# Kernel tuning notes

Hardware: AMD Instinct MI355X
Metric: run time of the kernel (lower is better)

The kernel has to match this reference:

```python
import jax, jax.numpy as jnp
import numpy as np

N_NODES, N_EDGES = 16384, 8192
IN_CH, HID_CH = 256, 256
ALPHA, BETA = -1.5, -0.5


def setup_inputs() -> dict:
    key = jax.random.key(0)
    k1, k2, k3, k4, k5, k6 = jax.random.split(key, 6)
    x_0 = jax.random.normal(k1, (N_NODES, IN_CH), dtype=jnp.float32)
    # binary incidence matrix (n_nodes, n_edges)
    incidence_1 = jax.random.randint(k2, (N_NODES, N_EDGES), 0, 2).astype(jnp.float32)
    # conv weights (torch Conv: x @ W then neighborhood @ .)
    W0 = jax.random.normal(k3, (IN_CH, HID_CH), dtype=jnp.float32) * 0.02
    W1 = jax.random.normal(k4, (HID_CH, HID_CH), dtype=jnp.float32) * 0.02
    # xavier_uniform biases of shape (1, hidden)
    gain = 1.414
    bound = gain * np.sqrt(6.0 / (1 + HID_CH)) * np.sqrt(3.0) / np.sqrt(3.0)  # xavier bound = gain*sqrt(6/(fan_in+fan_out))
    bound = gain * np.sqrt(6.0 / (1 + HID_CH))
    bias_0_to_1 = jax.random.uniform(k5, (1, HID_CH), minval=-bound, maxval=bound, dtype=jnp.float32)
    bias_1_to_0 = jax.random.uniform(k6, (1, HID_CH), minval=-bound, maxval=bound, dtype=jnp.float32)
    return {"x_0": x_0, "incidence_1": incidence_1, "W0": W0, "W1": W1,
            "bias_0_to_1": bias_0_to_1, "bias_1_to_0": bias_1_to_0}


def _normalize_incidence(B1):
    # edge/node cardinalities raised to alpha/beta
    edge_card = jnp.sum(B1, axis=0) ** ALPHA          # (n_edges,)
    node_card = jnp.sum(B1, axis=1) ** BETA           # (n_nodes,)
    mask = (B1 > 0).astype(B1.dtype)
    d0_inv = 1.0 / (mask @ edge_card)                 # (n_nodes,) per-node sum of incident edge_card
    d1_inv = 1.0 / (mask.T @ node_card)               # (n_edges,) per-edge sum of member node_card
    # B1_norm = D0_left^-1 @ B1 @ diag(edge_card)
    B1_norm = d0_inv[:, None] * B1 * edge_card[None, :]
    # B1T_norm = D1_left^-1 @ B1^T @ diag(node_card)
    B1T_norm = d1_inv[:, None] * B1.T * node_card[None, :]
    return B1_norm, B1T_norm


def reference(x_0, incidence_1, W0, W1, bias_0_to_1, bias_1_to_0):
    B1_norm, B1T_norm = _normalize_incidence(incidence_1)
    # node -> edge conv: x_1 = B1T_norm @ (x_0 @ W0) + b01
    x_1 = B1T_norm @ (x_0 @ W0) + bias_0_to_1        # (n_edges, hid)
    # edge -> node conv: x_0 = B1_norm @ (x_1 @ W1) + b10
    x_0_out = B1_norm @ (x_1 @ W1) + bias_1_to_0     # (n_nodes, hid)
    return jax.nn.relu(x_0_out), jax.nn.relu(x_1)
```

## Files before the change

kernel.cpp:

```cpp
#include <hip/hip_runtime.h>
#include <stdint.h>

#define NN 16384
#define NE 8192
#define CH 256
#define MM1_SPLIT 8
#define MM2_SPLIT 4

typedef __attribute__((ext_vector_type(8))) short bf16x8;
typedef __attribute__((ext_vector_type(4))) float f32x4;

__device__ __forceinline__ unsigned short f2bf(float f) {
  unsigned u = __float_as_uint(f);
  u += 0x7FFFu + ((u >> 16) & 1u);
  return (unsigned short)(u >> 16);
}
__device__ __forceinline__ unsigned pack_trunc2(float a, float b) {
  return (__float_as_uint(b) & 0xFFFF0000u) | (__float_as_uint(a) >> 16);
}
__device__ __forceinline__ void async_copy16(const void* gptr, void* lptr) {
  __builtin_amdgcn_global_load_lds((const __attribute__((address_space(1))) unsigned int*)gptr,
                                   (__attribute__((address_space(3))) unsigned int*)lptr,
                                   16, 0, 0);
}

__global__ void k0_transpose_w(const float* __restrict__ W0, const float* __restrict__ W1,
                               unsigned short* __restrict__ W0T, unsigned short* __restrict__ W1T) {
  const float* W = blockIdx.y ? W1 : W0;
  unsigned short* WT = blockIdx.y ? W1T : W0T;
  int n = blockIdx.x;
  int k = threadIdx.x;
  WT[n * CH + k] = f2bf(W[k * CH + n]);
}

__global__ void k0z_zero(float* __restrict__ rowsum) {
  rowsum[blockIdx.x * 256 + threadIdx.x] = 0.f;
}

__global__ __launch_bounds__(256) void k1_prep(const float* __restrict__ B1,
                                               unsigned short* __restrict__ b1h,
                                               unsigned short* __restrict__ b1hT,
                                               float* __restrict__ rowsum) {
  __shared__ unsigned short t16[128 * 136];
  __shared__ float rs[128][9];
  const int tid = threadIdx.x;
  const int e0 = blockIdx.x * 128;
  const int n0 = blockIdx.y * 128;
  const int rr = tid >> 3;
  const int ec = (tid & 7) * 16;
  float part[4];
#pragma unroll
  for (int rg = 0; rg < 4; ++rg) {
    int r = rg * 32 + rr;
    const float* src = B1 + (size_t)(n0 + r) * NE + e0 + ec;
    float s = 0.f;
    unsigned w[8];
#pragma unroll
    for (int u = 0; u < 4; ++u) {
      float4 v = *(const float4*)(src + u * 4);
      s += v.x + v.y + v.z + v.w;
      w[u * 2] = pack_trunc2(v.x, v.y);
      w[u * 2 + 1] = pack_trunc2(v.z, v.w);
    }
    part[rg] = s;
    uint4* d = (uint4*)(b1h + (size_t)(n0 + r) * NE + e0 + ec);
    d[0] = make_uint4(w[0], w[1], w[2], w[3]);
    d[1] = make_uint4(w[4], w[5], w[6], w[7]);
    unsigned* lp = (unsigned*)&t16[r * 136 + ec];
#pragma unroll
    for (int u = 0; u < 8; ++u) lp[u] = w[u];
  }
#pragma unroll
  for (int rg = 0; rg < 4; ++rg) rs[rg * 32 + rr][tid & 7] = part[rg];
  __syncthreads();
  if (tid < 128) {
    float s = 0.f;
#pragma unroll
    for (int u = 0; u < 8; ++u) s += rs[tid][u];
    atomicAdd(rowsum + n0 + tid, s);
  }
  const int p = tid & 63, h = tid >> 6;
  unsigned lo[16], hi[16];
#pragma unroll
  for (int u = 0; u < 16; ++u) {
    int n = h * 32 + u * 2;
    unsigned a = *(const unsigned*)&t16[n * 136 + p * 2];
    unsigned b = *(const unsigned*)&t16[(n + 1) * 136 + p * 2];
    lo[u] = (a & 0xFFFFu) | (b << 16);
    hi[u] = (a >> 16) | (b & 0xFFFF0000u);
  }
  uint4* d0 = (uint4*)(b1hT + (size_t)(e0 + 2 * p) * NN + n0 + h * 32);
  d0[0] = make_uint4(lo[0], lo[1], lo[2], lo[3]);
  d0[1] = make_uint4(lo[4], lo[5], lo[6], lo[7]);
  d0[2] = make_uint4(lo[8], lo[9], lo[10], lo[11]);
  d0[3] = make_uint4(lo[12], lo[13], lo[14], lo[15]);
  uint4* d1 = (uint4*)(b1hT + (size_t)(e0 + 2 * p + 1) * NN + n0 + h * 32);
  d1[0] = make_uint4(hi[0], hi[1], hi[2], hi[3]);
  d1[1] = make_uint4(hi[4], hi[5], hi[6], hi[7]);
  d1[2] = make_uint4(hi[8], hi[9], hi[10], hi[11]);
  d1[3] = make_uint4(hi[12], hi[13], hi[14], hi[15]);
}

__global__ void k1b_nc(const float* __restrict__ rowsum, float* __restrict__ node_card) {
  int n = blockIdx.x * 256 + threadIdx.x;
  node_card[n] = rsqrtf(rowsum[n]);
}

__global__ __launch_bounds__(256) void k2_y0(const float* __restrict__ X0,
                                             const unsigned short* __restrict__ W0T,
                                             const float* __restrict__ node_card,
                                             unsigned short* __restrict__ y0sT) {
  __shared__ unsigned short a_lds[64 * 32];
  __shared__ unsigned short b_lds[256 * 32];
  const int tid = threadIdx.x;
  const int wave = tid >> 6, lane = tid & 63;
  const int quad = lane >> 4, l15 = lane & 15;
  const int m0 = blockIdx.x * 64;
  const int ar = tid >> 3, ac = (tid & 7) * 4;

  f32x4 acc[4][4];
  const f32x4 fz = {0.f, 0.f, 0.f, 0.f};
#pragma unroll
  for (int i = 0; i < 4; ++i)
#pragma unroll
    for (int j = 0; j < 4; ++j) acc[i][j] = fz;

  for (int k0 = 0; k0 < CH; k0 += 32) {
    __syncthreads();
#pragma unroll
    for (int p = 0; p < 2; ++p) {
      float4 v = *(const float4*)(X0 + (size_t)(m0 + ar + p * 32) * CH + k0 + ac);
      uint2 w;
      w.x = ((unsigned)f2bf(v.x)) | ((unsigned)f2bf(v.y) << 16);
      w.y = ((unsigned)f2bf(v.z)) | ((unsigned)f2bf(v.w) << 16);
      *(uint2*)&a_lds[(ar + p * 32) * 32 + ac] = w;
    }
#pragma unroll
    for (int i = 0; i < 4; ++i) {
      int rowbase = wave * 64 + i * 16;
      const unsigned short* g = W0T + (size_t)(rowbase + (lane >> 2)) * CH + k0 + (lane & 3) * 8;
      async_copy16(g, &b_lds[rowbase * 32]);
    }
    __syncthreads();
    bf16x8 af[4];
#pragma unroll
    for (int i = 0; i < 4; ++i)
      af[i] = *(const bf16x8*)&a_lds[(i * 16 + l15) * 32 + quad * 8];
#pragma unroll
    for (int j = 0; j < 4; ++j) {
      bf16x8 bfr = *(const bf16x8*)&b_lds[(wave * 64 + j * 16 + l15) * 32 + quad * 8];
#pragma unroll
      for (int i = 0; i < 4; ++i)
        acc[i][j] = __builtin_amdgcn_mfma_f32_16x16x32_bf16(af[i], bfr, acc[i][j], 0, 0, 0);
    }
  }
#pragma unroll
  for (int i = 0; i < 4; ++i) {
    int row4 = m0 + i * 16 + quad * 4;
    float4 nc = *(const float4*)(node_card + row4);
#pragma unroll
    for (int j = 0; j < 4; ++j) {
      int col = wave * 64 + j * 16 + l15;
      f32x4 v = acc[i][j];
      ushort4 o;
      o.x = f2bf(v[0] * nc.x);
      o.y = f2bf(v[1] * nc.y);
      o.z = f2bf(v[2] * nc.z);
      o.w = f2bf(v[3] * nc.w);
      *(ushort4*)&y0sT[(size_t)col * NN + row4] = o;
    }
  }
}

__global__ void k2b_aux(const float* __restrict__ node_card, unsigned short* __restrict__ y0sT) {
  int n = blockIdx.x * 256 + threadIdx.x;
  y0sT[(size_t)256 * NN + n] = f2bf(node_card[n]);
  y0sT[(size_t)257 * NN + n] = 0x3F80;
#pragma unroll
  for (int r = 258; r < 272; ++r) y0sT[(size_t)r * NN + n] = 0;
}

template <int NSZ, int SPLIT>
__device__ __forceinline__ void mm_core(const unsigned short* __restrict__ Y,
                                        const unsigned short* __restrict__ Bm,
                                        float* __restrict__ outp) {
  constexpr int K = (NSZ == NE) ? NN : NE;
  constexpr int KS = K / SPLIT;
  constexpr int ITERS = KS / 64;
  __shared__ unsigned short a_lds[2][2][80][32];
  __shared__ unsigned short b_lds[2][2][128][32];
  const int tid = threadIdx.x;
  const int wave = tid >> 6, lane = tid & 63;
  const int quad = lane >> 4, l15 = lane & 15;
  const int bid = blockIdx.x;
  const int sp = bid % SPLIT;
  const int rest = bid / SPLIT;
  const int mq = rest & 3;
  const int nb = rest >> 2;
  const int n0 = nb * 128;
  const int mbase = mq * 64;
  const int MQ = (mq == 3) ? 5 : 4;
  const int kbase = sp * KS;
  const int lrow = lane >> 2;
  const int src_off = (((lane & 3) - ((lane >> 3) & 3)) & 3) * 8;
  const int qpos = (quad + ((l15 >> 1) & 3)) & 3;

  f32x4 acc[5][2];
  const f32x4 fz = {0.f, 0.f, 0.f, 0.f};
#pragma unroll
  for (int m = 0; m < 5; ++m)
#pragma unroll
    for (int j = 0; j < 2; ++j) acc[m][j] = fz;

  auto stage = [&](int buf, int k0) {
    for (int g = wave; g < MQ; g += 4) {
#pragma unroll
      for (int kh = 0; kh < 2; ++kh) {
        const unsigned short* src =
            Y + (size_t)(mbase + g * 16 + lrow) * K + k0 + kh * 32 + src_off;
        async_copy16(src, &a_lds[buf][kh][g * 16][0]);
      }
    }
#pragma unroll
    for (int gg = 0; gg < 2; ++gg) {
      int g = wave * 2 + gg;
#pragma unroll
      for (int kh = 0; kh < 2; ++kh) {
        const unsigned short* src =
            Bm + (size_t)(n0 + g * 16 + lrow) * K + k0 + kh * 32 + src_off;
        async_copy16(src, &b_lds[buf][kh][g * 16][0]);
      }
    }
  };

  stage(0, kbase);
  for (int i = 0; i < ITERS; ++i) {
    __syncthreads();
    if (i + 1 < ITERS) stage((i + 1) & 1, kbase + (i + 1) * 64);
    const int buf = i & 1;
#pragma unroll
    for (int kh = 0; kh < 2; ++kh) {
      bf16x8 af[5], bfr[2];
#pragma unroll
      for (int m = 0; m < 5; ++m)
        if (m < MQ) af[m] = *(const bf16x8*)&a_lds[buf][kh][m * 16 + l15][qpos * 8];
#pragma unroll
      for (int j = 0; j < 2; ++j)
        bfr[j] = *(const bf16x8*)&b_lds[buf][kh][wave * 32 + j * 16 + l15][qpos * 8];
#pragma unroll
      for (int m = 0; m < 5; ++m)
        if (m < MQ)
#pragma unroll
          for (int j = 0; j < 2; ++j)
            acc[m][j] = __builtin_amdgcn_mfma_f32_16x16x32_bf16(af[m], bfr[j], acc[m][j], 0, 0, 0);
    }
  }
  float* op = outp + (size_t)sp * 272 * NSZ;
#pragma unroll
  for (int m = 0; m < 5; ++m) {
    if (m < MQ) {
      int c0 = mbase + m * 16 + quad * 4;
#pragma unroll
      for (int j = 0; j < 2; ++j) {
        int n = n0 + wave * 32 + j * 16 + l15;
#pragma unroll
        for (int r = 0; r < 4; ++r) op[(size_t)(c0 + r) * NSZ + n] = acc[m][j][r];
      }
    }
  }
}

__global__ __launch_bounds__(256) void mm1t_kernel(const unsigned short* __restrict__ y0sT,
                                                   const unsigned short* __restrict__ b1hT,
                                                   float* __restrict__ mm1pT) {
  mm_core<NE, MM1_SPLIT>(y0sT, b1hT, mm1pT);
}
__global__ __launch_bounds__(256) void mm2t_kernel(const unsigned short* __restrict__ y1sT,
                                                   const unsigned short* __restrict__ b1h,
                                                   float* __restrict__ mm2pT) {
  mm_core<NN, MM2_SPLIT>(y1sT, b1h, mm2pT);
}

__global__ __launch_bounds__(256) void k3_edge_final(const float* __restrict__ mm1pT,
                                                     const float* __restrict__ b01,
                                                     float* __restrict__ out1,
                                                     unsigned short* __restrict__ x1bf,
                                                     float* __restrict__ edge_card) {
  __shared__ float tile[32 * 260];
  __shared__ float d1s[32], css[32];
  const int tid = threadIdx.x;
  const int e0 = blockIdx.x * 32;
  float p[32];
#pragma unroll
  for (int u = 0; u < 32; ++u) p[u] = 0.f;
  for (int sp = 0; sp < MM1_SPLIT; ++sp) {
    const float4* rp = (const float4*)(mm1pT + ((size_t)sp * 272 + tid) * NE + e0);
#pragma unroll
    for (int u = 0; u < 8; ++u) {
      float4 v = rp[u];
      p[u * 4 + 0] += v.x; p[u * 4 + 1] += v.y; p[u * 4 + 2] += v.z; p[u * 4 + 3] += v.w;
    }
  }
  if (tid < 64) {
    int row = 256 + (tid >> 5), e = e0 + (tid & 31);
    float s = 0.f;
    for (int sp = 0; sp < MM1_SPLIT; ++sp) s += mm1pT[((size_t)sp * 272 + row) * NE + e];
    if (tid < 32) d1s[tid] = s; else css[tid & 31] = s;
  }
  __syncthreads();
  float bc = b01[tid];
#pragma unroll
  for (int u = 0; u < 32; ++u) tile[u * 260 + tid] = p[u] / d1s[u] + bc;
  if (tid < 32) {
    float cs = css[tid];
    edge_card[e0 + tid] = 1.0f / (cs * sqrtf(cs));
  }
  __syncthreads();
  const int e = tid >> 3, cb = (tid & 7) * 32;
  const float* trow = &tile[e * 260 + cb];
  float* orow = out1 + (size_t)(e0 + e) * CH + cb;
  unsigned short* xrow = x1bf + (size_t)(e0 + e) * CH + cb;
#pragma unroll
  for (int v = 0; v < 32; v += 4) {
    float4 x;
    x.x = trow[v]; x.y = trow[v + 1]; x.z = trow[v + 2]; x.w = trow[v + 3];
    float4 rl;
    rl.x = fmaxf(x.x, 0.f); rl.y = fmaxf(x.y, 0.f); rl.z = fmaxf(x.z, 0.f); rl.w = fmaxf(x.w, 0.f);
    *(float4*)&orow[v] = rl;
    ushort4 h;
    h.x = f2bf(x.x); h.y = f2bf(x.y); h.z = f2bf(x.z); h.w = f2bf(x.w);
    *(ushort4*)&xrow[v] = h;
  }
}

__global__ __launch_bounds__(256) void k5_y1(const unsigned short* __restrict__ x1bf,
                                             const unsigned short* __restrict__ W1T,
                                             const float* __restrict__ edge_card,
                                             unsigned short* __restrict__ y1sT) {
  __shared__ unsigned short a_lds[64 * 32];
  __shared__ unsigned short b_lds[256 * 32];
  const int tid = threadIdx.x;
  const int wave = tid >> 6, lane = tid & 63;
  const int quad = lane >> 4, l15 = lane & 15;
  const int m0 = blockIdx.x * 64;

  f32x4 acc[4][4];
  const f32x4 fz = {0.f, 0.f, 0.f, 0.f};
#pragma unroll
  for (int i = 0; i < 4; ++i)
#pragma unroll
    for (int j = 0; j < 4; ++j) acc[i][j] = fz;

  for (int k0 = 0; k0 < CH; k0 += 32) {
    __syncthreads();
    {
      const unsigned short* g = x1bf + (size_t)(m0 + wave * 16 + (lane >> 2)) * CH + k0 + (lane & 3) * 8;
      async_copy16(g, &a_lds[(wave * 16) * 32]);
    }
#pragma unroll
    for (int i = 0; i < 4; ++i) {
      int rowbase = wave * 64 + i * 16;
      const unsigned short* g = W1T + (size_t)(rowbase + (lane >> 2)) * CH + k0 + (lane & 3) * 8;
      async_copy16(g, &b_lds[rowbase * 32]);
    }
    __syncthreads();
    bf16x8 af[4];
#pragma unroll
    for (int i = 0; i < 4; ++i)
      af[i] = *(const bf16x8*)&a_lds[(i * 16 + l15) * 32 + quad * 8];
#pragma unroll
    for (int j = 0; j < 4; ++j) {
      bf16x8 bfr = *(const bf16x8*)&b_lds[(wave * 64 + j * 16 + l15) * 32 + quad * 8];
#pragma unroll
      for (int i = 0; i < 4; ++i)
        acc[i][j] = __builtin_amdgcn_mfma_f32_16x16x32_bf16(af[i], bfr, acc[i][j], 0, 0, 0);
    }
  }
#pragma unroll
  for (int i = 0; i < 4; ++i) {
    int row4 = m0 + i * 16 + quad * 4;
    float4 ec = *(const float4*)(edge_card + row4);
#pragma unroll
    for (int j = 0; j < 4; ++j) {
      int col = wave * 64 + j * 16 + l15;
      f32x4 v = acc[i][j];
      ushort4 o;
      o.x = f2bf(v[0] * ec.x);
      o.y = f2bf(v[1] * ec.y);
      o.z = f2bf(v[2] * ec.z);
      o.w = f2bf(v[3] * ec.w);
      *(ushort4*)&y1sT[(size_t)col * NE + row4] = o;
    }
  }
}

__global__ void k5b_aux(const float* __restrict__ edge_card, unsigned short* __restrict__ y1sT) {
  int e = blockIdx.x * 256 + threadIdx.x;
  y1sT[(size_t)256 * NE + e] = f2bf(edge_card[e]);
#pragma unroll
  for (int r = 257; r < 272; ++r) y1sT[(size_t)r * NE + e] = 0;
}

__global__ __launch_bounds__(256) void k6_node_final(const float* __restrict__ mm2pT,
                                                     const float* __restrict__ b10,
                                                     float* __restrict__ out0) {
  __shared__ float tile[32 * 260];
  __shared__ float d0s[32];
  const int tid = threadIdx.x;
  const int n0 = blockIdx.x * 32;
  float p[32];
#pragma unroll
  for (int u = 0; u < 32; ++u) p[u] = 0.f;
  for (int sp = 0; sp < MM2_SPLIT; ++sp) {
    const float4* rp = (const float4*)(mm2pT + ((size_t)sp * 272 + tid) * NN + n0);
#pragma unroll
    for (int u = 0; u < 8; ++u) {
      float4 v = rp[u];
      p[u * 4 + 0] += v.x; p[u * 4 + 1] += v.y; p[u * 4 + 2] += v.z; p[u * 4 + 3] += v.w;
    }
  }
  if (tid < 32) {
    float s = 0.f;
    for (int sp = 0; sp < MM2_SPLIT; ++sp) s += mm2pT[((size_t)sp * 272 + 256) * NN + n0 + tid];
    d0s[tid] = s;
  }
  __syncthreads();
  float bc = b10[tid];
#pragma unroll
  for (int u = 0; u < 32; ++u) tile[u * 260 + tid] = p[u] / d0s[u] + bc;
  __syncthreads();
  const int n = tid >> 3, cb = (tid & 7) * 32;
  const float* trow = &tile[n * 260 + cb];
  float* orow = out0 + (size_t)(n0 + n) * CH + cb;
#pragma unroll
  for (int v = 0; v < 32; v += 4) {
    float4 x;
    x.x = trow[v]; x.y = trow[v + 1]; x.z = trow[v + 2]; x.w = trow[v + 3];
    float4 rl;
    rl.x = fmaxf(x.x, 0.f); rl.y = fmaxf(x.y, 0.f); rl.z = fmaxf(x.z, 0.f); rl.w = fmaxf(x.w, 0.f);
    *(float4*)&orow[v] = rl;
  }
}

extern "C" void kernel_launch(void* const* d_in, const int* in_sizes, int n_in,
                              void* d_out, int out_size, void* d_ws, size_t ws_size,
                              hipStream_t stream) {
  const float* x0 = (const float*)d_in[0];
  const float* B1 = (const float*)d_in[1];
  const float* W0 = (const float*)d_in[2];
  const float* W1 = (const float*)d_in[3];
  const float* b01 = (const float*)d_in[4];
  const float* b10 = (const float*)d_in[5];
  float* out0 = (float*)d_out;
  float* out1 = out0 + (size_t)NN * CH;

  char* ws = (char*)d_ws;
  size_t off = 0;
  auto take = [&](size_t bytes) {
    void* p = ws + off;
    off += (bytes + 255) & ~(size_t)255;
    return p;
  };
  unsigned short* b1h = (unsigned short*)take((size_t)NN * NE * 2);
  unsigned short* b1hT = (unsigned short*)take((size_t)NN * NE * 2);
  unsigned short* y0sT = (unsigned short*)take((size_t)272 * NN * 2);
  unsigned short* y1sT = (unsigned short*)take((size_t)272 * NE * 2);
  unsigned short* x1bf = (unsigned short*)take((size_t)NE * CH * 2);
  float* mm1pT = (float*)take((size_t)MM1_SPLIT * 272 * NE * 4);
  float* mm2pT = mm1pT;
  float* rowsum = (float*)take((size_t)NN * 4);
  float* node_card = (float*)take((size_t)NN * 4);
  float* edge_card = (float*)take((size_t)NE * 4);
  unsigned short* W0T = (unsigned short*)take((size_t)CH * CH * 2);
  unsigned short* W1T = (unsigned short*)take((size_t)CH * CH * 2);
  (void)ws_size; (void)in_sizes; (void)n_in; (void)out_size;

  k0_transpose_w<<<dim3(256, 2), 256, 0, stream>>>(W0, W1, W0T, W1T);
  k0z_zero<<<NN / 256, 256, 0, stream>>>(rowsum);
  k1_prep<<<dim3(NE / 128, NN / 128), 256, 0, stream>>>(B1, b1h, b1hT, rowsum);
  k1b_nc<<<NN / 256, 256, 0, stream>>>(rowsum, node_card);
  k2_y0<<<NN / 64, 256, 0, stream>>>(x0, W0T, node_card, y0sT);
  k2b_aux<<<NN / 256, 256, 0, stream>>>(node_card, y0sT);
  mm1t_kernel<<<(NE / 128) * 4 * MM1_SPLIT, 256, 0, stream>>>(y0sT, b1hT, mm1pT);
  k3_edge_final<<<NE / 32, 256, 0, stream>>>(mm1pT, b01, out1, x1bf, edge_card);
  k5_y1<<<NE / 64, 256, 0, stream>>>(x1bf, W1T, edge_card, y1sT);
  k5b_aux<<<NE / 256, 256, 0, stream>>>(edge_card, y1sT);
  mm2t_kernel<<<(NN / 128) * 4 * MM2_SPLIT, 256, 0, stream>>>(y1sT, b1h, mm2pT);
  k6_node_final<<<NN / 32, 256, 0, stream>>>(mm2pT, b10, out0);
}
```

Measured before the change: 1.148 ms.

## Load matmul operands straight to registers and read fp32 incidence directly in mm2

The LDS-staged matmul core is replaced by a register-prefetching version in which each wave loads its A and B fragments straight from global memory, with 2- and 4-deep prefetch. Tiles grow to 128 or 144 output channels and the split-K factors are halved. mm2 now reads the original fp32 incidence matrix and truncates it to bf16 in registers, so the bf16 copy b1h no longer has to be written. Small kernels are also folded away: the rowsum zeroing moves into the weight transpose and the rsqrt is computed inline. The risks are uncoalesced fragment loads, mm2 reading twice the bytes for B, and higher register pressure.

```diff
diff --git a/kernel.cpp b/kernel.cpp
--- a/kernel.cpp
+++ b/kernel.cpp
@@ -4,8 +4,8 @@
 #define NN 16384
 #define NE 8192
 #define CH 256
-#define MM1_SPLIT 8
-#define MM2_SPLIT 4
+#define MM1_SPLIT 4
+#define MM2_SPLIT 2
 
 typedef __attribute__((ext_vector_type(8))) short bf16x8;
 typedef __attribute__((ext_vector_type(4))) float f32x4;
@@ -25,20 +25,17 @@
 }
 
 __global__ void k0_transpose_w(const float* __restrict__ W0, const float* __restrict__ W1,
-                               unsigned short* __restrict__ W0T, unsigned short* __restrict__ W1T) {
+                               unsigned short* __restrict__ W0T, unsigned short* __restrict__ W1T,
+                               float* __restrict__ rowsum) {
   const float* W = blockIdx.y ? W1 : W0;
   unsigned short* WT = blockIdx.y ? W1T : W0T;
   int n = blockIdx.x;
   int k = threadIdx.x;
   WT[n * CH + k] = f2bf(W[k * CH + n]);
-}
-
-__global__ void k0z_zero(float* __restrict__ rowsum) {
-  rowsum[blockIdx.x * 256 + threadIdx.x] = 0.f;
+  if (blockIdx.y == 0 && blockIdx.x < NN / 256) rowsum[blockIdx.x * 256 + threadIdx.x] = 0.f;
 }
 
 __global__ __launch_bounds__(256) void k1_prep(const float* __restrict__ B1,
-                                               unsigned short* __restrict__ b1h,
                                                unsigned short* __restrict__ b1hT,
                                                float* __restrict__ rowsum) {
   __shared__ unsigned short t16[128 * 136];
@@ -63,9 +60,6 @@
       w[u * 2 + 1] = pack_trunc2(v.z, v.w);
     }
     part[rg] = s;
-    uint4* d = (uint4*)(b1h + (size_t)(n0 + r) * NE + e0 + ec);
-    d[0] = make_uint4(w[0], w[1], w[2], w[3]);
-    d[1] = make_uint4(w[4], w[5], w[6], w[7]);
     unsigned* lp = (unsigned*)&t16[r * 136 + ec];
 #pragma unroll
     for (int u = 0; u < 8; ++u) lp[u] = w[u];
@@ -101,14 +95,9 @@
   d1[3] = make_uint4(hi[12], hi[13], hi[14], hi[15]);
 }
 
-__global__ void k1b_nc(const float* __restrict__ rowsum, float* __restrict__ node_card) {
-  int n = blockIdx.x * 256 + threadIdx.x;
-  node_card[n] = rsqrtf(rowsum[n]);
-}
-
 __global__ __launch_bounds__(256) void k2_y0(const float* __restrict__ X0,
                                              const unsigned short* __restrict__ W0T,
-                                             const float* __restrict__ node_card,
+                                             const float* __restrict__ rowsum,
                                              unsigned short* __restrict__ y0sT) {
   __shared__ unsigned short a_lds[64 * 32];
   __shared__ unsigned short b_lds[256 * 32];
@@ -157,7 +146,9 @@
 #pragma unroll
   for (int i = 0; i < 4; ++i) {
     int row4 = m0 + i * 16 + quad * 4;
-    float4 nc = *(const float4*)(node_card + row4);
+    float4 rsv = *(const float4*)(rowsum + row4);
+    float4 nc;
+    nc.x = rsqrtf(rsv.x); nc.y = rsqrtf(rsv.y); nc.z = rsqrtf(rsv.z); nc.w = rsqrtf(rsv.w);
 #pragma unroll
     for (int j = 0; j < 4; ++j) {
       int col = wave * 64 + j * 16 + l15;
@@ -172,113 +163,137 @@
   }
 }
 
-__global__ void k2b_aux(const float* __restrict__ node_card, unsigned short* __restrict__ y0sT) {
+__global__ void k2b_aux(const float* __restrict__ rowsum, unsigned short* __restrict__ y0sT) {
   int n = blockIdx.x * 256 + threadIdx.x;
-  y0sT[(size_t)256 * NN + n] = f2bf(node_card[n]);
+  y0sT[(size_t)256 * NN + n] = f2bf(rsqrtf(rowsum[n]));
   y0sT[(size_t)257 * NN + n] = 0x3F80;
 #pragma unroll
   for (int r = 258; r < 272; ++r) y0sT[(size_t)r * NN + n] = 0;
 }
 
-template <int NSZ, int SPLIT>
-__device__ __forceinline__ void mm_core(const unsigned short* __restrict__ Y,
-                                        const unsigned short* __restrict__ Bm,
-                                        float* __restrict__ outp) {
-  constexpr int K = (NSZ == NE) ? NN : NE;
+template <int K, int NSZ, int SPLIT, bool F32S>
+__device__ __forceinline__ void mm_core_reg(const unsigned short* __restrict__ Y,
+                                            const void* __restrict__ BmV,
+                                            float* __restrict__ outp,
+                                            int sp, int mb, int nb) {
   constexpr int KS = K / SPLIT;
-  constexpr int ITERS = KS / 64;
-  __shared__ unsigned short a_lds[2][2][80][32];
-  __shared__ unsigned short b_lds[2][2][128][32];
+  constexpr int STEPS = KS / 32;
   const int tid = threadIdx.x;
   const int wave = tid >> 6, lane = tid & 63;
   const int quad = lane >> 4, l15 = lane & 15;
+  const int TM = mb ? 8 : 9, mtb = mb ? 9 : 0;
+  const int n0 = nb * 128 + wave * 32;
+  const int kb0 = sp * KS;
+  const char* Yb = (const char*)Y;
+  const char* Bb = (const char*)BmV;
+
+  f32x4 acc[9][2];
+  const f32x4 fz = {0.f, 0.f, 0.f, 0.f};
+#pragma unroll
+  for (int i = 0; i < 9; ++i)
+#pragma unroll
+    for (int j = 0; j < 2; ++j) acc[i][j] = fz;
+
+  unsigned voffA[9];
+#pragma unroll
+  for (int i = 0; i < 9; ++i)
+    voffA[i] = (unsigned)(((mtb + i) * 16 + l15) * K) * 2u + quad * 16;
+  unsigned voffB[2];
+#pragma unroll
+  for (int j = 0; j < 2; ++j) {
+    unsigned row = (unsigned)(n0 + j * 16 + l15);
+    voffB[j] = F32S ? (row * (unsigned)K * 4u + quad * 32) : (row * (unsigned)K * 2u + quad * 16);
+  }
+
+  bf16x8 Ar[2][9];
+  float4 Brf[4][2][2];
+  bf16x8 Brh[4][2];
+
+  auto loadA = [&](int it, int slot) {
+    unsigned kb = (unsigned)(kb0 + it * 32) * 2u;
+#pragma unroll
+    for (int i = 0; i < 9; ++i)
+      if (i < TM) Ar[slot][i] = *(const bf16x8*)(Yb + voffA[i] + kb);
+  };
+  auto loadB = [&](int it, int slot) {
+    if constexpr (F32S) {
+      unsigned kb = (unsigned)(kb0 + it * 32) * 4u;
+#pragma unroll
+      for (int j = 0; j < 2; ++j) {
+        Brf[slot][j][0] = *(const float4*)(Bb + voffB[j] + kb);
+        Brf[slot][j][1] = *(const float4*)(Bb + voffB[j] + kb + 16);
+      }
+    } else {
+      unsigned kb = (unsigned)(kb0 + it * 32) * 2u;
+#pragma unroll
+      for (int j = 0; j < 2; ++j) Brh[slot][j] = *(const bf16x8*)(Bb + voffB[j] + kb);
+    }
+  };
+
+#pragma unroll
+  for (int p = 0; p < 4; ++p) loadB(p, p);
+#pragma unroll
+  for (int p = 0; p < 2; ++p) loadA(p, p);
+
+#pragma unroll 4
+  for (int it = 0; it < STEPS; ++it) {
+    const int as = it & 1, bs = it & 3;
+#pragma unroll
+    for (int j = 0; j < 2; ++j) {
+      bf16x8 bj;
+      if constexpr (F32S) {
+        const unsigned* u = (const unsigned*)&Brf[bs][j][0];
+        unsigned w[4];
+        w[0] = (u[0] >> 16) | (u[1] & 0xFFFF0000u);
+        w[1] = (u[2] >> 16) | (u[3] & 0xFFFF0000u);
+        w[2] = (u[4] >> 16) | (u[5] & 0xFFFF0000u);
+        w[3] = (u[6] >> 16) | (u[7] & 0xFFFF0000u);
+        bj = *(const bf16x8*)w;
+      } else {
+        bj = Brh[bs][j];
+      }
+#pragma unroll
+      for (int i = 0; i < 9; ++i)
+        if (i < TM) acc[i][j] = __builtin_amdgcn_mfma_f32_16x16x32_bf16(Ar[as][i], bj, acc[i][j], 0, 0, 0);
+    }
+    int ita = it + 2; if (ita >= STEPS) ita = STEPS - 1;
+    loadA(ita, as);
+    int itb = it + 4; if (itb >= STEPS) itb = STEPS - 1;
+    loadB(itb, bs);
+  }
+
+  float* op = outp + (size_t)sp * 272 * NSZ;
+#pragma unroll
+  for (int i = 0; i < 9; ++i) {
+    if (i < TM) {
+      int c0 = (mtb + i) * 16 + quad * 4;
+#pragma unroll
+      for (int j = 0; j < 2; ++j) {
+        int n = n0 + j * 16 + l15;
+#pragma unroll
+        for (int r = 0; r < 4; ++r) op[(size_t)(c0 + r) * NSZ + n] = acc[i][j][r];
+      }
+    }
+  }
+}
+
+__global__ __launch_bounds__(256, 2) void mm1t_kernel(const unsigned short* __restrict__ y0sT,
+                                                      const unsigned short* __restrict__ b1hT,
+                                                      float* __restrict__ mm1pT) {
   const int bid = blockIdx.x;
-  const int sp = bid % SPLIT;
-  const int rest = bid / SPLIT;
-  const int mq = rest & 3;
-  const int nb = rest >> 2;
-  const int n0 = nb * 128;
-  const int mbase = mq * 64;
-  const int MQ = (mq == 3) ? 5 : 4;
-  const int kbase = sp * KS;
-  const int lrow = lane >> 2;
-  const int src_off = (((lane & 3) - ((lane >> 3) & 3)) & 3) * 8;
-  const int qpos = (quad + ((l15 >> 1) & 3)) & 3;
-
-  f32x4 acc[5][2];
-  const f32x4 fz = {0.f, 0.f, 0.f, 0.f};
-#pragma unroll
-  for (int m = 0; m < 5; ++m)
-#pragma unroll
-    for (int j = 0; j < 2; ++j) acc[m][j] = fz;
-
-  auto stage = [&](int buf, int k0) {
-    for (int g = wave; g < MQ; g += 4) {
-#pragma unroll
-      for (int kh = 0; kh < 2; ++kh) {
-        const unsigned short* src =
-            Y + (size_t)(mbase + g * 16 + lrow) * K + k0 + kh * 32 + src_off;
-        async_copy16(src, &a_lds[buf][kh][g * 16][0]);
-      }
-    }
-#pragma unroll
-    for (int gg = 0; gg < 2; ++gg) {
-      int g = wave * 2 + gg;
-#pragma unroll
-      for (int kh = 0; kh < 2; ++kh) {
-        const unsigned short* src =
-            Bm + (size_t)(n0 + g * 16 + lrow) * K + k0 + kh * 32 + src_off;
-        async_copy16(src, &b_lds[buf][kh][g * 16][0]);
-      }
-    }
-  };
-
-  stage(0, kbase);
-  for (int i = 0; i < ITERS; ++i) {
-    __syncthreads();
-    if (i + 1 < ITERS) stage((i + 1) & 1, kbase + (i + 1) * 64);
-    const int buf = i & 1;
-#pragma unroll
-    for (int kh = 0; kh < 2; ++kh) {
-      bf16x8 af[5], bfr[2];
-#pragma unroll
-      for (int m = 0; m < 5; ++m)
-        if (m < MQ) af[m] = *(const bf16x8*)&a_lds[buf][kh][m * 16 + l15][qpos * 8];
-#pragma unroll
-      for (int j = 0; j < 2; ++j)
-        bfr[j] = *(const bf16x8*)&b_lds[buf][kh][wave * 32 + j * 16 + l15][qpos * 8];
-#pragma unroll
-      for (int m = 0; m < 5; ++m)
-        if (m < MQ)
-#pragma unroll
-          for (int j = 0; j < 2; ++j)
-            acc[m][j] = __builtin_amdgcn_mfma_f32_16x16x32_bf16(af[m], bfr[j], acc[m][j], 0, 0, 0);
-    }
-  }
-  float* op = outp + (size_t)sp * 272 * NSZ;
-#pragma unroll
-  for (int m = 0; m < 5; ++m) {
-    if (m < MQ) {
-      int c0 = mbase + m * 16 + quad * 4;
-#pragma unroll
-      for (int j = 0; j < 2; ++j) {
-        int n = n0 + wave * 32 + j * 16 + l15;
-#pragma unroll
-        for (int r = 0; r < 4; ++r) op[(size_t)(c0 + r) * NSZ + n] = acc[m][j][r];
-      }
-    }
-  }
-}
-
-__global__ __launch_bounds__(256) void mm1t_kernel(const unsigned short* __restrict__ y0sT,
-                                                   const unsigned short* __restrict__ b1hT,
-                                                   float* __restrict__ mm1pT) {
-  mm_core<NE, MM1_SPLIT>(y0sT, b1hT, mm1pT);
-}
-__global__ __launch_bounds__(256) void mm2t_kernel(const unsigned short* __restrict__ y1sT,
-                                                   const unsigned short* __restrict__ b1h,
-                                                   float* __restrict__ mm2pT) {
-  mm_core<NN, MM2_SPLIT>(y1sT, b1h, mm2pT);
+  const int sp = bid & 3;
+  const int mb = (bid >> 3) & 1;
+  const int nb = ((bid >> 2) & 1) + 2 * (bid >> 4);
+  mm_core_reg<NN, NE, MM1_SPLIT, false>(y0sT, b1hT, mm1pT, sp, mb, nb);
+}
+__global__ __launch_bounds__(256, 2) void mm2t_kernel(const unsigned short* __restrict__ y1sT,
+                                                      const float* __restrict__ B1,
+                                                      float* __restrict__ mm2pT) {
+  const int bid = blockIdx.x;
+  const int sp = bid & 1;
+  const int mb = (bid >> 3) & 1;
+  const int nb = ((bid >> 1) & 3) + 4 * (bid >> 4);
+  mm_core_reg<NE, NN, MM2_SPLIT, true>(y1sT, B1, mm2pT, sp, mb, nb);
 }
 
 __global__ __launch_bounds__(256) void k3_edge_final(const float* __restrict__ mm1pT,
@@ -461,7 +476,6 @@
     off += (bytes + 255) & ~(size_t)255;
     return p;
   };
-  unsigned short* b1h = (unsigned short*)take((size_t)NN * NE * 2);
   unsigned short* b1hT = (unsigned short*)take((size_t)NN * NE * 2);
   unsigned short* y0sT = (unsigned short*)take((size_t)272 * NN * 2);
   unsigned short* y1sT = (unsigned short*)take((size_t)272 * NE * 2);
@@ -469,22 +483,19 @@
   float* mm1pT = (float*)take((size_t)MM1_SPLIT * 272 * NE * 4);
   float* mm2pT = mm1pT;
   float* rowsum = (float*)take((size_t)NN * 4);
-  float* node_card = (float*)take((size_t)NN * 4);
   float* edge_card = (float*)take((size_t)NE * 4);
   unsigned short* W0T = (unsigned short*)take((size_t)CH * CH * 2);
   unsigned short* W1T = (unsigned short*)take((size_t)CH * CH * 2);
   (void)ws_size; (void)in_sizes; (void)n_in; (void)out_size;
 
-  k0_transpose_w<<<dim3(256, 2), 256, 0, stream>>>(W0, W1, W0T, W1T);
-  k0z_zero<<<NN / 256, 256, 0, stream>>>(rowsum);
-  k1_prep<<<dim3(NE / 128, NN / 128), 256, 0, stream>>>(B1, b1h, b1hT, rowsum);
-  k1b_nc<<<NN / 256, 256, 0, stream>>>(rowsum, node_card);
-  k2_y0<<<NN / 64, 256, 0, stream>>>(x0, W0T, node_card, y0sT);
-  k2b_aux<<<NN / 256, 256, 0, stream>>>(node_card, y0sT);
-  mm1t_kernel<<<(NE / 128) * 4 * MM1_SPLIT, 256, 0, stream>>>(y0sT, b1hT, mm1pT);
+  k0_transpose_w<<<dim3(256, 2), 256, 0, stream>>>(W0, W1, W0T, W1T, rowsum);
+  k1_prep<<<dim3(NE / 128, NN / 128), 256, 0, stream>>>(B1, b1hT, rowsum);
+  k2_y0<<<NN / 64, 256, 0, stream>>>(x0, W0T, rowsum, y0sT);
+  k2b_aux<<<NN / 256, 256, 0, stream>>>(rowsum, y0sT);
+  mm1t_kernel<<<(NE / 128) * 2 * MM1_SPLIT, 256, 0, stream>>>(y0sT, b1hT, mm1pT);
   k3_edge_final<<<NE / 32, 256, 0, stream>>>(mm1pT, b01, out1, x1bf, edge_card);
   k5_y1<<<NE / 64, 256, 0, stream>>>(x1bf, W1T, edge_card, y1sT);
   k5b_aux<<<NE / 256, 256, 0, stream>>>(edge_card, y1sT);
-  mm2t_kernel<<<(NN / 128) * 4 * MM2_SPLIT, 256, 0, stream>>>(y1sT, b1h, mm2pT);
+  mm2t_kernel<<<(NN / 128) * 2 * MM2_SPLIT, 256, 0, stream>>>(y1sT, B1, mm2pT);
   k6_node_final<<<NN / 32, 256, 0, stream>>>(mm2pT, b10, out0);
 }
```

Result: slower. 1.525 ms (+32.8%).
